# Kernel tuning notes

Measured on AMD Instinct MI355X. Metric: run time of the kernel, lower is better.

## Reference

```python
import jax, jax.numpy as jnp
import numpy as np

B, N, D = 16, 4096, 6
NUM_CENTERS, K = 1024, 32
EPS = 1e-5


def setup_inputs() -> dict:
    key = jax.random.key(0)
    ks = jax.random.split(key, 6)
    xyz = jax.random.uniform(ks[0], (B, N, 3), dtype=jnp.float32)
    features = jax.random.normal(ks[1], (B, N, D), dtype=jnp.float32)
    W1 = jax.random.normal(ks[2], (3 + D, 64), dtype=jnp.float32) * 0.1
    W2 = jax.random.normal(ks[3], (64, 64), dtype=jnp.float32) * 0.1
    W3 = jax.random.normal(ks[4], (64, 128), dtype=jnp.float32) * 0.1
    return {
        "xyz": xyz, "features": features,
        "W1": W1, "g1": jnp.ones((64,)), "b1": jnp.zeros((64,)),
        "W2": W2, "g2": jnp.ones((64,)), "b2": jnp.zeros((64,)),
        "W3": W3, "g3": jnp.ones((128,)), "b3": jnp.zeros((128,)),
    }


def square_distance(a, b):
    # a: [B,S,3], b: [B,N,3] -> [B,S,N] squared euclidean distance
    d2 = (jnp.sum(a * a, -1)[:, :, None]
          + jnp.sum(b * b, -1)[:, None, :]
          - 2.0 * jnp.einsum('bsc,bnc->bsn', a, b))
    return jnp.maximum(d2, 0.0)


def farthest_point_sample(xyz, num_centers):
    # xyz: [B,N,3] -> centers_idx: [B,S]. First center fixed at index 0
    # (original uses a random first index; deterministic here).
    Bn = xyz.shape[0]
    batch = jnp.arange(Bn)
    first = jnp.zeros((Bn,), jnp.int32)
    d0 = jnp.sum((xyz - xyz[batch, first][:, None, :]) ** 2, -1)  # [B,N]

    def step(dist_closest, _):
        idx = jnp.argmax(dist_closest, axis=1).astype(jnp.int32)  # [B]
        c = xyz[batch, idx]                                        # [B,3]
        d = jnp.sum((xyz - c[:, None, :]) ** 2, -1)                # [B,N]
        return jnp.minimum(dist_closest, d), idx

    _, rest = jax.lax.scan(step, d0, None, length=num_centers - 1)  # [S-1,B]
    return jnp.concatenate([first[:, None], rest.T], axis=1)        # [B,S]


def gather_bsk(points, idx):
    # points: [B,N,C], idx: [B,S,K] -> [B,S,K,C]
    Bn = points.shape[0]
    return points[jnp.arange(Bn)[:, None, None], idx]


def conv_bn_relu(x, W, g, b):
    # 1x1 conv (channel matmul) + training-mode BatchNorm (biased var) + ReLU
    x = jnp.einsum('bskc,co->bsko', x, W)
    m = jnp.mean(x, axis=(0, 1, 2))
    v = jnp.var(x, axis=(0, 1, 2))
    return jax.nn.relu((x - m) * jax.lax.rsqrt(v + EPS) * g + b)


def reference(xyz, features, W1, g1, b1, W2, g2, b2, W3, g3, b3):
    Bn = xyz.shape[0]
    batch = jnp.arange(Bn)
    centers_idx = farthest_point_sample(xyz, NUM_CENTERS)          # [B,S]
    centers_xyz = xyz[batch[:, None], centers_idx]                  # [B,S,3]

    # kNN grouping: [B,S,N] distance matrix, top-K smallest
    d2 = square_distance(centers_xyz, xyz)
    _, group_idx = jax.lax.top_k(-d2, K)                            # [B,S,K]

    group_xyz = gather_bsk(xyz, group_idx) - centers_xyz[:, :, None, :]
    group_feat = gather_bsk(features, group_idx)
    group = jnp.concatenate([group_xyz, group_feat], axis=-1)       # [B,S,K,3+D]

    x = conv_bn_relu(group, W1, g1, b1)
    x = conv_bn_relu(x, W2, g2, b2)
    x = conv_bn_relu(x, W3, g3, b3)
    centers_features = jnp.max(x, axis=2)                           # [B,S,C_out]
    return centers_xyz, centers_features
```

## Files before the change

kernel.cpp:

```cpp
#include <hip/hip_runtime.h>

#define BN_   16
#define NPTS  4096
#define DFEAT 6
#define SCTR  1024
#define KNN   32
#define RTOT  (BN_*SCTR*KNN)
#define EPSV  1e-5f
#define RNF   524288.0f
#define NREP  64

__device__ __forceinline__ float fmulx(float a, float b){ return __fmul_rn(a,b); }
__device__ __forceinline__ float faddx(float a, float b){ return __fadd_rn(a,b); }
__device__ __forceinline__ float fsubx(float a, float b){ return __fsub_rn(a,b); }
__device__ __forceinline__ float sq3x(float x, float y, float z){
  return faddx(faddx(fmulx(x,x), fmulx(y,y)), fmulx(z,z));
}
__device__ __forceinline__ float dot3fma(float ax, float ay, float az,
                                         float bx, float by, float bz){
  return __fmaf_rn(az, bz, __fmaf_rn(ay, by, __fmul_rn(ax, bx)));
}

__device__ __forceinline__ unsigned fkey(float f){
  unsigned u = __float_as_uint(f);
  return (u & 0x80000000u) ? ~u : (u | 0x80000000u);
}
__device__ __forceinline__ float funkey(unsigned k){
  return (k & 0x80000000u) ? __uint_as_float(k & 0x7fffffffu) : __uint_as_float(~k);
}

template<int CTRL>
__device__ __forceinline__ unsigned dpp_mv(unsigned v){
  return (unsigned)__builtin_amdgcn_update_dpp((int)v, (int)v, CTRL, 0xf, 0xf, false);
}
__device__ __forceinline__ unsigned wave_umax_b(unsigned v){
  unsigned o;
  o=dpp_mv<0x111>(v); v=v>o?v:o;
  o=dpp_mv<0x112>(v); v=v>o?v:o;
  o=dpp_mv<0x114>(v); v=v>o?v:o;
  o=dpp_mv<0x118>(v); v=v>o?v:o;
  o=dpp_mv<0x142>(v); v=v>o?v:o;
  o=dpp_mv<0x143>(v); v=v>o?v:o;
  return (unsigned)__builtin_amdgcn_readlane((int)v, 63);
}
__device__ __forceinline__ unsigned wave_umin_b(unsigned v){
  unsigned o;
  o=dpp_mv<0x111>(v); v=v<o?v:o;
  o=dpp_mv<0x112>(v); v=v<o?v:o;
  o=dpp_mv<0x114>(v); v=v<o?v:o;
  o=dpp_mv<0x118>(v); v=v<o?v:o;
  o=dpp_mv<0x142>(v); v=v<o?v:o;
  o=dpp_mv<0x143>(v); v=v<o?v:o;
  return (unsigned)__builtin_amdgcn_readlane((int)v, 63);
}

__global__ __launch_bounds__(256) void k_fps(const float* __restrict__ xyz,
                                             float* __restrict__ cxyz){
  const int b = blockIdx.x, tid = threadIdx.x;
  const int wave = tid>>6, lane = tid&63;
  const float* X = xyz + (size_t)b*NPTS*3;
  __shared__ float Xl[NPTS*3];
  __shared__ float Cl[SCTR*3];
  __shared__ unsigned long long slot[2][4];
  for(int i=tid;i<NPTS*3;i+=256) Xl[i]=X[i];
  __syncthreads();
  float px[16],py[16],pz[16],mind[16];
  const float c0x=Xl[0], c0y=Xl[1], c0z=Xl[2];
#pragma unroll
  for(int t=0;t<16;t++){
    const int j = lane + 64*(wave*16+t);
    px[t]=Xl[j*3]; py[t]=Xl[j*3+1]; pz[t]=Xl[j*3+2];
    mind[t]=sq3x(fsubx(px[t],c0x), fsubx(py[t],c0y), fsubx(pz[t],c0z));
  }
  if(tid==0){ Cl[0]=c0x; Cl[1]=c0y; Cl[2]=c0z; }
  float bv=-1.0f; int bj=0x7fffffff;
#pragma unroll
  for(int t=0;t<16;t++){
    const int j = lane + 64*(wave*16+t);
    if(mind[t]>bv){ bv=mind[t]; bj=j; }
  }
  for(int it=1; it<SCTR; ++it){
    const unsigned uv = __float_as_uint(bv);
    const unsigned M  = wave_umax_b(uv);
    const unsigned nj = (uv == M) ? ~(unsigned)bj : 0u;
    const unsigned NJ = wave_umax_b(nj);
    if(lane==0) slot[it&1][wave] = ((unsigned long long)M<<32) | NJ;
    __syncthreads();
    unsigned long long k0=slot[it&1][0], k1=slot[it&1][1],
                       k2=slot[it&1][2], k3=slot[it&1][3];
    unsigned long long ka = k0>k1?k0:k1;
    unsigned long long kb = k2>k3?k2:k3;
    unsigned long long kw = ka>kb?ka:kb;
    const int w = (int)(~(unsigned)kw);
    const float cx=Xl[w*3], cy=Xl[w*3+1], cz=Xl[w*3+2];
    if(tid==0){ Cl[it*3]=cx; Cl[it*3+1]=cy; Cl[it*3+2]=cz; }
    bv=-1.0f; bj=0x7fffffff;
#pragma unroll
    for(int t=0;t<16;t++){
      float d = sq3x(fsubx(px[t],cx), fsubx(py[t],cy), fsubx(pz[t],cz));
      float nm = fminf(mind[t], d);
      mind[t]=nm;
      const int j = lane + 64*(wave*16+t);
      if(nm>bv){ bv=nm; bj=j; }
    }
  }
  __syncthreads();
  float* O = cxyz + (size_t)b*SCTR*3;
  for(int i=tid;i<SCTR*3;i+=256) O[i]=Cl[i];
}

__global__ __launch_bounds__(256) void k_select(const float* __restrict__ xyz,
                                                const float* __restrict__ cxyz,
                                                int* __restrict__ gidx){
  const int lane = threadIdx.x & 63;
  const int cid  = blockIdx.x*4 + (threadIdx.x>>6);
  const int b = cid>>10;
  const float* X = xyz + (size_t)b*NPTS*3;
  const float* C = cxyz + (size_t)cid*3;
  const float cx=C[0], cy=C[1], cz=C[2];
  const float a2 = sq3x(cx,cy,cz);
  float d[64];
#pragma unroll
  for(int t=0;t<64;t++){
    int j = lane + (t<<6);
    float x=X[j*3], y=X[j*3+1], z=X[j*3+2];
    float b2 = sq3x(x,y,z);
    float dt = dot3fma(cx,cy,cz, x,y,z);
    float dd = fsubx(faddx(a2,b2), fmulx(2.0f,dt));
    d[t] = fmaxf(dd, 0.0f);
  }
  unsigned long long taken = 0ull;
  int* out = gidx + (size_t)cid*KNN;
#pragma unroll 1
  for(int r=0;r<KNN;r++){
    float mv = 3.0e38f; int mt = 63;
#pragma unroll
    for(int t=0;t<64;t++){
      if(!(taken & (1ull<<t)) && d[t] < mv){ mv = d[t]; mt = t; }
    }
    const unsigned um = __float_as_uint(mv);
    const unsigned Mw = wave_umin_b(um);
    const unsigned jc = (um == Mw) ? (unsigned)(lane + (mt<<6)) : 0xffffffffu;
    const unsigned WJ = wave_umin_b(jc);
    if(lane == (int)(WJ & 63u)){
      out[r] = (int)WJ;
      taken |= (1ull << (WJ >> 6));
    }
  }
}

__device__ __forceinline__ void stage_in(float* INt, int rbase,
                                         const float* __restrict__ xyz,
                                         const float* __restrict__ feat,
                                         const float* __restrict__ cxyz,
                                         const int* __restrict__ gidx){
  const int tid = threadIdx.x;
  const int row = tid>>2, sub = tid&3;
  const int r  = rbase + row;
  const int bb = r>>15, ss=(r>>5)&1023;
  const int idx = gidx[r];
  if(sub==0){
    const float* P = xyz  + ((size_t)bb*NPTS + idx)*3;
    const float* C = cxyz + ((size_t)(bb*SCTR)+ss)*3;
    INt[0*68+row] = P[0]-C[0];
    INt[1*68+row] = P[1]-C[1];
    INt[2*68+row] = P[2]-C[2];
  }else{
    const float* F = feat + ((size_t)bb*NPTS + idx)*6;
    const int c = (sub-1)*2;
    INt[(3+c)*68+row] = F[c];
    INt[(4+c)*68+row] = F[c+1];
  }
}

__device__ __forceinline__ void gemm1(const float* INt, const float* __restrict__ W1,
                                      int rt, int ct, float acc[4][4]){
#pragma unroll
  for(int i=0;i<4;i++)
#pragma unroll
    for(int j=0;j<4;j++) acc[i][j]=0.f;
#pragma unroll
  for(int c=0;c<9;c++){
    const float4 a = *(const float4*)&INt[c*68 + rt*4];
    const float4 w = *(const float4*)&W1[c*64 + ct*4];
    const float av[4]={a.x,a.y,a.z,a.w}, wv[4]={w.x,w.y,w.z,w.w};
#pragma unroll
    for(int i=0;i<4;i++)
#pragma unroll
      for(int j=0;j<4;j++) acc[i][j] += av[i]*wv[j];
  }
}

__device__ __forceinline__ float fold_rep(const float* __restrict__ pstats, int off){
  float s=0.f;
#pragma unroll 8
  for(int c=0;c<NREP;c++) s += pstats[c*512 + off];
  return s;
}

__global__ __launch_bounds__(256) void k_stats1(const float* __restrict__ xyz,
                                                const float* __restrict__ feat,
                                                const float* __restrict__ cxyz,
                                                const int* __restrict__ gidx,
                                                const float* __restrict__ W1,
                                                float* __restrict__ pstats){
  __shared__ __align__(16) float INt[9*68];
  __shared__ float sb[64], qb[64];
  const int tid=threadIdx.x;
  if(tid<64){ sb[tid]=0.f; qb[tid]=0.f; }
  stage_in(INt, blockIdx.x*64, xyz, feat, cxyz, gidx);
  __syncthreads();
  const int rt=tid&15, ct=tid>>4;
  float acc[4][4];
  gemm1(INt, W1, rt, ct, acc);
#pragma unroll
  for(int j=0;j<4;j++){
    float s=0.f, q=0.f;
#pragma unroll
    for(int i=0;i<4;i++){ float v=acc[i][j]; s+=v; q+=v*v; }
    atomicAdd(&sb[ct*4+j], s); atomicAdd(&qb[ct*4+j], q);
  }
  __syncthreads();
  if(tid<64){
    float* ps = pstats + (size_t)(blockIdx.x & (NREP-1))*512;
    atomicAdd(&ps[tid], sb[tid]); atomicAdd(&ps[64+tid], qb[tid]);
  }
}

template<bool WRITEZ>
__device__ __forceinline__ void stats2_body(const float* xyz, const float* feat,
                                            const float* cxyz, const int* gidx,
                                            const float* W1, const float* g1,
                                            const float* b1, const float* __restrict__ W2,
                                            float* pstats, float* Z2){
  __shared__ __align__(16) float INt[9*68];
  __shared__ __align__(16) float A1t[64*68];
  __shared__ float af1A[64], af1B[64];
  __shared__ float sb[64], qb[64];
  const int tid=threadIdx.x;
  if(tid<64){
    float sm = fold_rep(pstats, tid);
    float sq = fold_rep(pstats, 64+tid);
    float m  = sm/RNF;
    float vv = sq/RNF - m*m;
    float A  = rsqrtf(vv+EPSV)*g1[tid];
    af1A[tid]=A; af1B[tid]=b1[tid]-m*A;
    sb[tid]=0.f; qb[tid]=0.f;
  }
  stage_in(INt, blockIdx.x*64, xyz, feat, cxyz, gidx);
  __syncthreads();
  const int rt=tid&15, ct=tid>>4;
  float acc1[4][4];
  gemm1(INt, W1, rt, ct, acc1);
#pragma unroll
  for(int j=0;j<4;j++){
    const int o=ct*4+j; const float A=af1A[o], Bc=af1B[o];
#pragma unroll
    for(int i=0;i<4;i++) A1t[o*68 + rt*4+i] = fmaxf(acc1[i][j]*A+Bc, 0.f);
  }
  __syncthreads();
  float acc2[4][4];
#pragma unroll
  for(int i=0;i<4;i++)
#pragma unroll
    for(int j=0;j<4;j++) acc2[i][j]=0.f;
#pragma unroll
  for(int c=0;c<64;c++){
    const float4 a = *(const float4*)&A1t[c*68 + rt*4];
    const float4 w = *(const float4*)&W2[c*64 + ct*4];
    const float av[4]={a.x,a.y,a.z,a.w}, wv[4]={w.x,w.y,w.z,w.w};
#pragma unroll
    for(int i=0;i<4;i++)
#pragma unroll
      for(int j=0;j<4;j++) acc2[i][j] += av[i]*wv[j];
  }
  if(WRITEZ){
#pragma unroll
    for(int i=0;i<4;i++){
      float4 v = make_float4(acc2[i][0],acc2[i][1],acc2[i][2],acc2[i][3]);
      *(float4*)&Z2[((size_t)blockIdx.x*64 + rt*4+i)*64 + ct*4] = v;
    }
  }
#pragma unroll
  for(int j=0;j<4;j++){
    float s=0.f, q=0.f;
#pragma unroll
    for(int i=0;i<4;i++){ float v=acc2[i][j]; s+=v; q+=v*v; }
    atomicAdd(&sb[ct*4+j], s); atomicAdd(&qb[ct*4+j], q);
  }
  __syncthreads();
  if(tid<64){
    float* ps = pstats + (size_t)(blockIdx.x & (NREP-1))*512;
    atomicAdd(&ps[128+tid], sb[tid]); atomicAdd(&ps[192+tid], qb[tid]);
  }
}

__global__ __launch_bounds__(256) void k_stats2(const float* __restrict__ xyz,
                                                const float* __restrict__ feat,
                                                const float* __restrict__ cxyz,
                                                const int* __restrict__ gidx,
                                                const float* __restrict__ W1,
                                                const float* __restrict__ g1,
                                                const float* __restrict__ b1,
                                                const float* __restrict__ W2,
                                                float* __restrict__ pstats){
  stats2_body<false>(xyz,feat,cxyz,gidx,W1,g1,b1,W2,pstats,nullptr);
}
__global__ __launch_bounds__(256) void k_stats2m(const float* __restrict__ xyz,
                                                 const float* __restrict__ feat,
                                                 const float* __restrict__ cxyz,
                                                 const int* __restrict__ gidx,
                                                 const float* __restrict__ W1,
                                                 const float* __restrict__ g1,
                                                 const float* __restrict__ b1,
                                                 const float* __restrict__ W2,
                                                 float* __restrict__ pstats,
                                                 float* __restrict__ Z2){
  stats2_body<true>(xyz,feat,cxyz,gidx,W1,g1,b1,W2,pstats,Z2);
}

__global__ __launch_bounds__(256) void k_layer3(const float* __restrict__ xyz,
                                                const float* __restrict__ feat,
                                                const float* __restrict__ cxyz,
                                                const int* __restrict__ gidx,
                                                const float* __restrict__ W1,
                                                const float* __restrict__ g1,
                                                const float* __restrict__ b1,
                                                const float* __restrict__ W2,
                                                const float* __restrict__ g2,
                                                const float* __restrict__ b2,
                                                const float* __restrict__ W3,
                                                float* __restrict__ pstats,
                                                float* __restrict__ premax){
  __shared__ __align__(16) float INt[9*68];
  __shared__ __align__(16) float A1t[64*68];
  __shared__ float af1A[64], af1B[64], af2A[64], af2B[64];
  __shared__ unsigned mx[256];
  __shared__ float s3b[256], q3b[256];
  const int tid=threadIdx.x;
  if(tid<64){
    float sm = fold_rep(pstats, tid);
    float sq = fold_rep(pstats, 64+tid);
    float m  = sm/RNF;
    float vv = sq/RNF - m*m;
    float A  = rsqrtf(vv+EPSV)*g1[tid];
    af1A[tid]=A; af1B[tid]=b1[tid]-m*A;
    float sm2 = fold_rep(pstats, 128+tid);
    float sq2 = fold_rep(pstats, 192+tid);
    float m2 = sm2/RNF;
    float v2 = sq2/RNF - m2*m2;
    float A2 = rsqrtf(v2+EPSV)*g2[tid];
    af2A[tid]=A2; af2B[tid]=b2[tid]-m2*A2;
  }
  mx[tid]=0u; s3b[tid]=0.f; q3b[tid]=0.f;
  stage_in(INt, blockIdx.x*64, xyz, feat, cxyz, gidx);
  __syncthreads();
  const int rt=tid&15, ct=tid>>4;
  float acc1[4][4];
  gemm1(INt, W1, rt, ct, acc1);
#pragma unroll
  for(int j=0;j<4;j++){
    const int o=ct*4+j; const float A=af1A[o], Bc=af1B[o];
#pragma unroll
    for(int i=0;i<4;i++) A1t[o*68 + rt*4+i] = fmaxf(acc1[i][j]*A+Bc, 0.f);
  }
  __syncthreads();
  float acc2[4][4];
#pragma unroll
  for(int i=0;i<4;i++)
#pragma unroll
    for(int j=0;j<4;j++) acc2[i][j]=0.f;
#pragma unroll
  for(int c=0;c<64;c++){
    const float4 a = *(const float4*)&A1t[c*68 + rt*4];
    const float4 w = *(const float4*)&W2[c*64 + ct*4];
    const float av[4]={a.x,a.y,a.z,a.w}, wv[4]={w.x,w.y,w.z,w.w};
#pragma unroll
    for(int i=0;i<4;i++)
#pragma unroll
      for(int j=0;j<4;j++) acc2[i][j] += av[i]*wv[j];
  }
  float a2v[4][4];
#pragma unroll
  for(int j=0;j<4;j++){
    const int o=ct*4+j; const float A=af2A[o], Bc=af2B[o];
#pragma unroll
    for(int i=0;i<4;i++) a2v[i][j]=fmaxf(acc2[i][j]*A+Bc, 0.f);
  }
  __syncthreads();
#pragma unroll
  for(int j=0;j<4;j++)
#pragma unroll
    for(int i=0;i<4;i++) A1t[(ct*4+j)*68 + rt*4+i] = a2v[i][j];
  __syncthreads();
  float acc3[4][8];
#pragma unroll
  for(int i=0;i<4;i++)
#pragma unroll
    for(int j=0;j<8;j++) acc3[i][j]=0.f;
#pragma unroll
  for(int c=0;c<64;c++){
    const float4 a  = *(const float4*)&A1t[c*68 + rt*4];
    const float4 w0 = *(const float4*)&W3[c*128 + ct*8];
    const float4 w1 = *(const float4*)&W3[c*128 + ct*8 + 4];
    const float av[4]={a.x,a.y,a.z,a.w};
    const float wv[8]={w0.x,w0.y,w0.z,w0.w,w1.x,w1.y,w1.z,w1.w};
#pragma unroll
    for(int i=0;i<4;i++)
#pragma unroll
      for(int j=0;j<8;j++) acc3[i][j] += av[i]*wv[j];
  }
  const int g = rt>>3;
#pragma unroll
  for(int j=0;j<8;j++){
    const int o=ct*8+j;
    float lm=acc3[0][j], s=0.f, q=0.f;
#pragma unroll
    for(int i=0;i<4;i++){ float v=acc3[i][j]; lm=fmaxf(lm,v); s+=v; q+=v*v; }
    atomicMax(&mx[g*128+o], fkey(lm));
    atomicAdd(&s3b[g*128+o], s);
    atomicAdd(&q3b[g*128+o], q);
  }
  __syncthreads();
  {
    const int gg=tid>>7, o=tid&127;
    const int cid = blockIdx.x*2+gg;
    premax[(size_t)cid*128+o] = funkey(mx[tid]);
  }
  if(tid<128){
    float* ps = pstats + (size_t)(blockIdx.x & (NREP-1))*512;
    atomicAdd(&ps[256+tid], s3b[tid]+s3b[128+tid]);
    atomicAdd(&ps[384+tid], q3b[tid]+q3b[128+tid]);
  }
}

__global__ __launch_bounds__(256) void k_layer3z(const float* __restrict__ Z2,
                                                 const float* __restrict__ g2,
                                                 const float* __restrict__ b2,
                                                 const float* __restrict__ W3,
                                                 float* __restrict__ pstats,
                                                 float* __restrict__ premax){
  __shared__ __align__(16) float A2t[64*68];
  __shared__ float af2A[64], af2B[64];
  __shared__ unsigned mx[256];
  __shared__ float s3b[256], q3b[256];
  const int tid=threadIdx.x;
  if(tid<64){
    float sm2 = fold_rep(pstats, 128+tid);
    float sq2 = fold_rep(pstats, 192+tid);
    float m2 = sm2/RNF;
    float v2 = sq2/RNF - m2*m2;
    float A2 = rsqrtf(v2+EPSV)*g2[tid];
    af2A[tid]=A2; af2B[tid]=b2[tid]-m2*A2;
  }
  mx[tid]=0u; s3b[tid]=0.f; q3b[tid]=0.f;
  __syncthreads();
  {
    const int row = tid>>2, cq = (tid&3)*16;
    const float* zr = Z2 + ((size_t)blockIdx.x*64 + row)*64 + cq;
    const float4 z0 = *(const float4*)(zr);
    const float4 z1 = *(const float4*)(zr+4);
    const float4 z2 = *(const float4*)(zr+8);
    const float4 z3 = *(const float4*)(zr+12);
    const float zz[16]={z0.x,z0.y,z0.z,z0.w, z1.x,z1.y,z1.z,z1.w,
                        z2.x,z2.y,z2.z,z2.w, z3.x,z3.y,z3.z,z3.w};
#pragma unroll
    for(int u=0;u<16;u++){
      const int c = cq+u;
      A2t[c*68+row] = fmaxf(zz[u]*af2A[c]+af2B[c], 0.f);
    }
  }
  __syncthreads();
  const int rt=tid&15, ct=tid>>4;
  float acc3[4][8];
#pragma unroll
  for(int i=0;i<4;i++)
#pragma unroll
    for(int j=0;j<8;j++) acc3[i][j]=0.f;
#pragma unroll
  for(int c=0;c<64;c++){
    const float4 a  = *(const float4*)&A2t[c*68 + rt*4];
    const float4 w0 = *(const float4*)&W3[c*128 + ct*8];
    const float4 w1 = *(const float4*)&W3[c*128 + ct*8 + 4];
    const float av[4]={a.x,a.y,a.z,a.w};
    const float wv[8]={w0.x,w0.y,w0.z,w0.w,w1.x,w1.y,w1.z,w1.w};
#pragma unroll
    for(int i=0;i<4;i++)
#pragma unroll
      for(int j=0;j<8;j++) acc3[i][j] += av[i]*wv[j];
  }
  const int g = rt>>3;
#pragma unroll
  for(int j=0;j<8;j++){
    const int o=ct*8+j;
    float lm=acc3[0][j], s=0.f, q=0.f;
#pragma unroll
    for(int i=0;i<4;i++){ float v=acc3[i][j]; lm=fmaxf(lm,v); s+=v; q+=v*v; }
    atomicMax(&mx[g*128+o], fkey(lm));
    atomicAdd(&s3b[g*128+o], s);
    atomicAdd(&q3b[g*128+o], q);
  }
  __syncthreads();
  {
    const int gg=tid>>7, o=tid&127;
    const int cid = blockIdx.x*2+gg;
    premax[(size_t)cid*128+o] = funkey(mx[tid]);
  }
  if(tid<128){
    float* ps = pstats + (size_t)(blockIdx.x & (NREP-1))*512;
    atomicAdd(&ps[256+tid], s3b[tid]+s3b[128+tid]);
    atomicAdd(&ps[384+tid], q3b[tid]+q3b[128+tid]);
  }
}

__global__ __launch_bounds__(256) void k_red3(const float* __restrict__ pstats,
                                              float* __restrict__ cstats){
  const int t = threadIdx.x;
  cstats[t] = fold_rep(pstats, 256+t);
}

__global__ __launch_bounds__(256) void k_final(const float* __restrict__ cstats,
                                               const float* __restrict__ g3,
                                               const float* __restrict__ b3,
                                               float* __restrict__ outf){
  const int i = blockIdx.x*256 + threadIdx.x;
  const int o = i & 127;
  float m  = cstats[o]/RNF;
  float vv = cstats[128+o]/RNF - m*m;
  float A  = rsqrtf(vv+EPSV)*g3[o];
  float Bc = b3[o]-m*A;
  float v  = outf[i];
  outf[i] = fmaxf(v*A+Bc, 0.f);
}

extern "C" void kernel_launch(void* const* d_in, const int* in_sizes, int n_in,
                              void* d_out, int out_size, void* d_ws, size_t ws_size,
                              hipStream_t stream){
  const float* xyz  = (const float*)d_in[0];
  const float* feat = (const float*)d_in[1];
  const float* W1   = (const float*)d_in[2];
  const float* g1   = (const float*)d_in[3];
  const float* b1   = (const float*)d_in[4];
  const float* W2   = (const float*)d_in[5];
  const float* g2   = (const float*)d_in[6];
  const float* b2   = (const float*)d_in[7];
  const float* W3   = (const float*)d_in[8];
  const float* g3   = (const float*)d_in[9];
  const float* b3   = (const float*)d_in[10];
  float* out  = (float*)d_out;
  float* cxyz = out;
  float* outf = out + 16*1024*3;
  float* pstats = (float*)d_ws;
  float* cstats = (float*)((char*)d_ws + 131072);
  int*   gidx   = (int*)((char*)d_ws + 133120);
  float* Z2     = (float*)((char*)d_ws + 133120 + (size_t)RTOT*4);
  const size_t need = 133120 + (size_t)RTOT*4 + (size_t)RTOT*64*4;
  const bool fast = (ws_size >= need);

  hipMemsetAsync(pstats, 0, (size_t)NREP*512*sizeof(float), stream);
  k_fps   <<<16,   256,  0, stream>>>(xyz, cxyz);
  k_select<<<4096, 256,  0, stream>>>(xyz, cxyz, gidx);
  k_stats1<<<8192, 256,  0, stream>>>(xyz, feat, cxyz, gidx, W1, pstats);
  if(fast){
    k_stats2m<<<8192, 256, 0, stream>>>(xyz, feat, cxyz, gidx, W1, g1, b1, W2, pstats, Z2);
    k_layer3z<<<8192, 256, 0, stream>>>(Z2, g2, b2, W3, pstats, outf);
  }else{
    k_stats2 <<<8192, 256, 0, stream>>>(xyz, feat, cxyz, gidx, W1, g1, b1, W2, pstats);
    k_layer3 <<<8192, 256, 0, stream>>>(xyz, feat, cxyz, gidx, W1, g1, b1, W2, g2, b2, W3, pstats, outf);
  }
  k_red3  <<<1,    256,  0, stream>>>(pstats, cstats);
  k_final <<<8192, 256,  0, stream>>>(cstats, g3, b3, outf);
}
```

Baseline: 1.667 ms.

## Widen FPS to 512 threads and use quarter-cached minima in kNN selection

The farthest-point-sampling kernel now runs 8 waves per batch instead of 4, so each lane holds 8 points rather than 16 and the serial 1023-iteration loop does half the per-lane distance work, at the cost of an 8-way cross-wave reduction. The kNN selection kernel keeps a cached minimum for each of four 16-entry quarters of the per-lane distance array. Each round only compares those four values, and only the winning lane rescans the quarter it took from, instead of every lane scanning all 64 entries every round. This reduces per-round ALU work but adds divergent rescans and more register state.

```diff
diff --git a/kernel.cpp b/kernel.cpp
--- a/kernel.cpp
+++ b/kernel.cpp
@@ -54,29 +54,29 @@
   return (unsigned)__builtin_amdgcn_readlane((int)v, 63);
 }
 
-__global__ __launch_bounds__(256) void k_fps(const float* __restrict__ xyz,
+__global__ __launch_bounds__(512) void k_fps(const float* __restrict__ xyz,
                                              float* __restrict__ cxyz){
   const int b = blockIdx.x, tid = threadIdx.x;
   const int wave = tid>>6, lane = tid&63;
   const float* X = xyz + (size_t)b*NPTS*3;
   __shared__ float Xl[NPTS*3];
   __shared__ float Cl[SCTR*3];
-  __shared__ unsigned long long slot[2][4];
-  for(int i=tid;i<NPTS*3;i+=256) Xl[i]=X[i];
-  __syncthreads();
-  float px[16],py[16],pz[16],mind[16];
+  __shared__ unsigned long long slot[2][8];
+  for(int i=tid;i<NPTS*3;i+=512) Xl[i]=X[i];
+  __syncthreads();
+  float px[8],py[8],pz[8],mind[8];
   const float c0x=Xl[0], c0y=Xl[1], c0z=Xl[2];
 #pragma unroll
-  for(int t=0;t<16;t++){
-    const int j = lane + 64*(wave*16+t);
+  for(int t=0;t<8;t++){
+    const int j = lane + 64*(wave*8+t);
     px[t]=Xl[j*3]; py[t]=Xl[j*3+1]; pz[t]=Xl[j*3+2];
     mind[t]=sq3x(fsubx(px[t],c0x), fsubx(py[t],c0y), fsubx(pz[t],c0z));
   }
   if(tid==0){ Cl[0]=c0x; Cl[1]=c0y; Cl[2]=c0z; }
   float bv=-1.0f; int bj=0x7fffffff;
 #pragma unroll
-  for(int t=0;t<16;t++){
-    const int j = lane + 64*(wave*16+t);
+  for(int t=0;t<8;t++){
+    const int j = lane + 64*(wave*8+t);
     if(mind[t]>bv){ bv=mind[t]; bj=j; }
   }
   for(int it=1; it<SCTR; ++it){
@@ -86,27 +86,32 @@
     const unsigned NJ = wave_umax_b(nj);
     if(lane==0) slot[it&1][wave] = ((unsigned long long)M<<32) | NJ;
     __syncthreads();
-    unsigned long long k0=slot[it&1][0], k1=slot[it&1][1],
-                       k2=slot[it&1][2], k3=slot[it&1][3];
-    unsigned long long ka = k0>k1?k0:k1;
-    unsigned long long kb = k2>k3?k2:k3;
-    unsigned long long kw = ka>kb?ka:kb;
+    const unsigned long long* sp = slot[it&1];
+    const unsigned long long s0=sp[0], s1=sp[1], s2=sp[2], s3=sp[3],
+                             s4=sp[4], s5=sp[5], s6=sp[6], s7=sp[7];
+    unsigned long long ka = s0>s1?s0:s1;
+    unsigned long long kb = s2>s3?s2:s3;
+    unsigned long long kc = s4>s5?s4:s5;
+    unsigned long long kd = s6>s7?s6:s7;
+    unsigned long long ke = ka>kb?ka:kb;
+    unsigned long long kf = kc>kd?kc:kd;
+    unsigned long long kw = ke>kf?ke:kf;
     const int w = (int)(~(unsigned)kw);
     const float cx=Xl[w*3], cy=Xl[w*3+1], cz=Xl[w*3+2];
     if(tid==0){ Cl[it*3]=cx; Cl[it*3+1]=cy; Cl[it*3+2]=cz; }
     bv=-1.0f; bj=0x7fffffff;
 #pragma unroll
-    for(int t=0;t<16;t++){
-      float d = sq3x(fsubx(px[t],cx), fsubx(py[t],cy), fsubx(pz[t],cz));
-      float nm = fminf(mind[t], d);
+    for(int t=0;t<8;t++){
+      float dd = sq3x(fsubx(px[t],cx), fsubx(py[t],cy), fsubx(pz[t],cz));
+      float nm = fminf(mind[t], dd);
       mind[t]=nm;
-      const int j = lane + 64*(wave*16+t);
+      const int j = lane + 64*(wave*8+t);
       if(nm>bv){ bv=nm; bj=j; }
     }
   }
   __syncthreads();
   float* O = cxyz + (size_t)b*SCTR*3;
-  for(int i=tid;i<SCTR*3;i+=256) O[i]=Cl[i];
+  for(int i=tid;i<SCTR*3;i+=512) O[i]=Cl[i];
 }
 
 __global__ __launch_bounds__(256) void k_select(const float* __restrict__ xyz,
@@ -129,23 +134,49 @@
     float dd = fsubx(faddx(a2,b2), fmulx(2.0f,dt));
     d[t] = fmaxf(dd, 0.0f);
   }
+  float q0v=3.0e38f, q1v=3.0e38f, q2v=3.0e38f, q3v=3.0e38f;
+  int   q0t=0, q1t=16, q2t=32, q3t=48;
+#pragma unroll
+  for(int k=0;k<16;k++){ if(d[k]    < q0v){ q0v=d[k];    q0t=k;    } }
+#pragma unroll
+  for(int k=0;k<16;k++){ if(d[16+k] < q1v){ q1v=d[16+k]; q1t=16+k; } }
+#pragma unroll
+  for(int k=0;k<16;k++){ if(d[32+k] < q2v){ q2v=d[32+k]; q2t=32+k; } }
+#pragma unroll
+  for(int k=0;k<16;k++){ if(d[48+k] < q3v){ q3v=d[48+k]; q3t=48+k; } }
   unsigned long long taken = 0ull;
   int* out = gidx + (size_t)cid*KNN;
 #pragma unroll 1
   for(int r=0;r<KNN;r++){
-    float mv = 3.0e38f; int mt = 63;
-#pragma unroll
-    for(int t=0;t<64;t++){
-      if(!(taken & (1ull<<t)) && d[t] < mv){ mv = d[t]; mt = t; }
-    }
+    float mv = q0v; int mt = q0t;
+    if(q1v < mv){ mv=q1v; mt=q1t; }
+    if(q2v < mv){ mv=q2v; mt=q2t; }
+    if(q3v < mv){ mv=q3v; mt=q3t; }
     const unsigned um = __float_as_uint(mv);
     const unsigned Mw = wave_umin_b(um);
     const unsigned jc = (um == Mw) ? (unsigned)(lane + (mt<<6)) : 0xffffffffu;
     const unsigned WJ = wave_umin_b(jc);
-    if(lane == (int)(WJ & 63u)){
+    const int wl = (int)(WJ & 63u);
+    const int wt = (int)(WJ >> 6);
+    if(lane == wl){
       out[r] = (int)WJ;
-      taken |= (1ull << (WJ >> 6));
+      taken |= (1ull << wt);
     }
+    const int wq = wt >> 4;
+#define RESCAN_Q(QV,QT,BASE) \
+    if(lane == wl){ \
+      float nv=3.0e38f; int nt=BASE; \
+      _Pragma("unroll") \
+      for(int k2=0;k2<16;k2++){ \
+        if(!(taken & (1ull<<(BASE+k2))) && d[BASE+k2] < nv){ nv=d[BASE+k2]; nt=BASE+k2; } \
+      } \
+      QV=nv; QT=nt; \
+    }
+    if(wq==0)      { RESCAN_Q(q0v,q0t,0)  }
+    else if(wq==1) { RESCAN_Q(q1v,q1t,16) }
+    else if(wq==2) { RESCAN_Q(q2v,q2t,32) }
+    else           { RESCAN_Q(q3v,q3t,48) }
+#undef RESCAN_Q
   }
 }
 
@@ -558,7 +589,7 @@
   const bool fast = (ws_size >= need);
 
   hipMemsetAsync(pstats, 0, (size_t)NREP*512*sizeof(float), stream);
-  k_fps   <<<16,   256,  0, stream>>>(xyz, cxyz);
+  k_fps   <<<16,   512,  0, stream>>>(xyz, cxyz);
   k_select<<<4096, 256,  0, stream>>>(xyz, cxyz, gidx);
   k_stats1<<<8192, 256,  0, stream>>>(xyz, feat, cxyz, gidx, W1, pstats);
   if(fast){
```

Result: faster. 1.555 ms (-6.7%).

## Cache per-quarter minima in kNN select, DPP stat reductions, precompute BN coefficients

Applied to the files above, without the earlier changes.

The kNN selection now keeps four per-lane quarter minima and, after each pick, rescans only the quarter that lost an element. The old code rescanned all 64 candidates on every one of the 32 rounds. Per-block batch-norm sum and sum-of-squares reductions replace LDS atomics with DPP row reductions across the 16 row-threads. BN affine coefficients are computed once in a tiny k_coef kernel instead of every block folding 64 replicas of the partial stats. This adds two small kernel launches and a divergent rescan branch in the select loop.

```diff
diff --git a/kernel.cpp b/kernel.cpp
--- a/kernel.cpp
+++ b/kernel.cpp
@@ -52,6 +52,15 @@
   o=dpp_mv<0x142>(v); v=v<o?v:o;
   o=dpp_mv<0x143>(v); v=v<o?v:o;
   return (unsigned)__builtin_amdgcn_readlane((int)v, 63);
+}
+
+__device__ __forceinline__ float row16_sum(float x){
+  float s = x;
+  s += __int_as_float(__builtin_amdgcn_update_dpp(0, __float_as_int(s), 0x111, 0xf, 0xf, true));
+  s += __int_as_float(__builtin_amdgcn_update_dpp(0, __float_as_int(s), 0x112, 0xf, 0xf, true));
+  s += __int_as_float(__builtin_amdgcn_update_dpp(0, __float_as_int(s), 0x114, 0xf, 0xf, true));
+  s += __int_as_float(__builtin_amdgcn_update_dpp(0, __float_as_int(s), 0x118, 0xf, 0xf, true));
+  return s;
 }
 
 __global__ __launch_bounds__(256) void k_fps(const float* __restrict__ xyz,
@@ -129,23 +138,49 @@
     float dd = fsubx(faddx(a2,b2), fmulx(2.0f,dt));
     d[t] = fmaxf(dd, 0.0f);
   }
+  float q0v=3.0e38f, q1v=3.0e38f, q2v=3.0e38f, q3v=3.0e38f;
+  int   q0t=0, q1t=16, q2t=32, q3t=48;
+#pragma unroll
+  for(int k=0;k<16;k++){ if(d[k]    < q0v){ q0v=d[k];    q0t=k;    } }
+#pragma unroll
+  for(int k=0;k<16;k++){ if(d[16+k] < q1v){ q1v=d[16+k]; q1t=16+k; } }
+#pragma unroll
+  for(int k=0;k<16;k++){ if(d[32+k] < q2v){ q2v=d[32+k]; q2t=32+k; } }
+#pragma unroll
+  for(int k=0;k<16;k++){ if(d[48+k] < q3v){ q3v=d[48+k]; q3t=48+k; } }
   unsigned long long taken = 0ull;
   int* out = gidx + (size_t)cid*KNN;
 #pragma unroll 1
   for(int r=0;r<KNN;r++){
-    float mv = 3.0e38f; int mt = 63;
-#pragma unroll
-    for(int t=0;t<64;t++){
-      if(!(taken & (1ull<<t)) && d[t] < mv){ mv = d[t]; mt = t; }
-    }
+    float mv = q0v; int mt = q0t;
+    if(q1v < mv){ mv=q1v; mt=q1t; }
+    if(q2v < mv){ mv=q2v; mt=q2t; }
+    if(q3v < mv){ mv=q3v; mt=q3t; }
     const unsigned um = __float_as_uint(mv);
     const unsigned Mw = wave_umin_b(um);
     const unsigned jc = (um == Mw) ? (unsigned)(lane + (mt<<6)) : 0xffffffffu;
     const unsigned WJ = wave_umin_b(jc);
-    if(lane == (int)(WJ & 63u)){
+    const int wl = (int)(WJ & 63u);
+    const int wt = (int)(WJ >> 6);
+    if(lane == wl){
       out[r] = (int)WJ;
-      taken |= (1ull << (WJ >> 6));
+      taken |= (1ull << wt);
     }
+    const int wq = wt >> 4;
+#define RESCAN_Q(QV,QT,BASE) \
+    if(lane == wl){ \
+      float nv=3.0e38f; int nt=BASE; \
+      _Pragma("unroll") \
+      for(int k2=0;k2<16;k2++){ \
+        if(!(taken & (1ull<<(BASE+k2))) && d[BASE+k2] < nv){ nv=d[BASE+k2]; nt=BASE+k2; } \
+      } \
+      QV=nv; QT=nt; \
+    }
+    if(wq==0)      { RESCAN_Q(q0v,q0t,0)  }
+    else if(wq==1) { RESCAN_Q(q1v,q1t,16) }
+    else if(wq==2) { RESCAN_Q(q2v,q2t,32) }
+    else           { RESCAN_Q(q3v,q3t,48) }
+#undef RESCAN_Q
   }
 }
 
@@ -198,6 +233,21 @@
   return s;
 }
 
+__global__ __launch_bounds__(64) void k_coef(const float* __restrict__ pstats,
+                                             const float* __restrict__ g,
+                                             const float* __restrict__ b,
+                                             float* __restrict__ coefo,
+                                             int off){
+  const int t = threadIdx.x;
+  float sm = fold_rep(pstats, off+t);
+  float sq = fold_rep(pstats, off+64+t);
+  float m  = sm/RNF;
+  float vv = sq/RNF - m*m;
+  float A  = rsqrtf(vv+EPSV)*g[t];
+  coefo[t]    = A;
+  coefo[64+t] = b[t]-m*A;
+}
+
 __global__ __launch_bounds__(256) void k_stats1(const float* __restrict__ xyz,
                                                 const float* __restrict__ feat,
                                                 const float* __restrict__ cxyz,
@@ -207,7 +257,6 @@
   __shared__ __align__(16) float INt[9*68];
   __shared__ float sb[64], qb[64];
   const int tid=threadIdx.x;
-  if(tid<64){ sb[tid]=0.f; qb[tid]=0.f; }
   stage_in(INt, blockIdx.x*64, xyz, feat, cxyz, gidx);
   __syncthreads();
   const int rt=tid&15, ct=tid>>4;
@@ -218,7 +267,8 @@
     float s=0.f, q=0.f;
 #pragma unroll
     for(int i=0;i<4;i++){ float v=acc[i][j]; s+=v; q+=v*v; }
-    atomicAdd(&sb[ct*4+j], s); atomicAdd(&qb[ct*4+j], q);
+    s = row16_sum(s); q = row16_sum(q);
+    if(rt==15){ sb[ct*4+j]=s; qb[ct*4+j]=q; }
   }
   __syncthreads();
   if(tid<64){
@@ -230,8 +280,9 @@
 template<bool WRITEZ>
 __device__ __forceinline__ void stats2_body(const float* xyz, const float* feat,
                                             const float* cxyz, const int* gidx,
-                                            const float* W1, const float* g1,
-                                            const float* b1, const float* __restrict__ W2,
+                                            const float* W1,
+                                            const float* __restrict__ coef,
+                                            const float* __restrict__ W2,
                                             float* pstats, float* Z2){
   __shared__ __align__(16) float INt[9*68];
   __shared__ __align__(16) float A1t[64*68];
@@ -239,13 +290,7 @@
   __shared__ float sb[64], qb[64];
   const int tid=threadIdx.x;
   if(tid<64){
-    float sm = fold_rep(pstats, tid);
-    float sq = fold_rep(pstats, 64+tid);
-    float m  = sm/RNF;
-    float vv = sq/RNF - m*m;
-    float A  = rsqrtf(vv+EPSV)*g1[tid];
-    af1A[tid]=A; af1B[tid]=b1[tid]-m*A;
-    sb[tid]=0.f; qb[tid]=0.f;
+    af1A[tid]=coef[tid]; af1B[tid]=coef[64+tid];
   }
   stage_in(INt, blockIdx.x*64, xyz, feat, cxyz, gidx);
   __syncthreads();
@@ -286,7 +331,8 @@
     float s=0.f, q=0.f;
 #pragma unroll
     for(int i=0;i<4;i++){ float v=acc2[i][j]; s+=v; q+=v*v; }
-    atomicAdd(&sb[ct*4+j], s); atomicAdd(&qb[ct*4+j], q);
+    s = row16_sum(s); q = row16_sum(q);
+    if(rt==15){ sb[ct*4+j]=s; qb[ct*4+j]=q; }
   }
   __syncthreads();
   if(tid<64){
@@ -300,23 +346,21 @@
                                                 const float* __restrict__ cxyz,
                                                 const int* __restrict__ gidx,
                                                 const float* __restrict__ W1,
-                                                const float* __restrict__ g1,
-                                                const float* __restrict__ b1,
+                                                const float* __restrict__ coef,
                                                 const float* __restrict__ W2,
                                                 float* __restrict__ pstats){
-  stats2_body<false>(xyz,feat,cxyz,gidx,W1,g1,b1,W2,pstats,nullptr);
+  stats2_body<false>(xyz,feat,cxyz,gidx,W1,coef,W2,pstats,nullptr);
 }
 __global__ __launch_bounds__(256) void k_stats2m(const float* __restrict__ xyz,
                                                  const float* __restrict__ feat,
                                                  const float* __restrict__ cxyz,
                                                  const int* __restrict__ gidx,
                                                  const float* __restrict__ W1,
-                                                 const float* __restrict__ g1,
-                                                 const float* __restrict__ b1,
+                                                 const float* __restrict__ coef,
                                                  const float* __restrict__ W2,
                                                  float* __restrict__ pstats,
                                                  float* __restrict__ Z2){
-  stats2_body<true>(xyz,feat,cxyz,gidx,W1,g1,b1,W2,pstats,Z2);
+  stats2_body<true>(xyz,feat,cxyz,gidx,W1,coef,W2,pstats,Z2);
 }
 
 __global__ __launch_bounds__(256) void k_layer3(const float* __restrict__ xyz,
@@ -324,11 +368,8 @@
                                                 const float* __restrict__ cxyz,
                                                 const int* __restrict__ gidx,
                                                 const float* __restrict__ W1,
-                                                const float* __restrict__ g1,
-                                                const float* __restrict__ b1,
+                                                const float* __restrict__ coef,
                                                 const float* __restrict__ W2,
-                                                const float* __restrict__ g2,
-                                                const float* __restrict__ b2,
                                                 const float* __restrict__ W3,
                                                 float* __restrict__ pstats,
                                                 float* __restrict__ premax){
@@ -336,23 +377,13 @@
   __shared__ __align__(16) float A1t[64*68];
   __shared__ float af1A[64], af1B[64], af2A[64], af2B[64];
   __shared__ unsigned mx[256];
-  __shared__ float s3b[256], q3b[256];
+  __shared__ float s3b[128], q3b[128];
   const int tid=threadIdx.x;
   if(tid<64){
-    float sm = fold_rep(pstats, tid);
-    float sq = fold_rep(pstats, 64+tid);
-    float m  = sm/RNF;
-    float vv = sq/RNF - m*m;
-    float A  = rsqrtf(vv+EPSV)*g1[tid];
-    af1A[tid]=A; af1B[tid]=b1[tid]-m*A;
-    float sm2 = fold_rep(pstats, 128+tid);
-    float sq2 = fold_rep(pstats, 192+tid);
-    float m2 = sm2/RNF;
-    float v2 = sq2/RNF - m2*m2;
-    float A2 = rsqrtf(v2+EPSV)*g2[tid];
-    af2A[tid]=A2; af2B[tid]=b2[tid]-m2*A2;
-  }
-  mx[tid]=0u; s3b[tid]=0.f; q3b[tid]=0.f;
+    af1A[tid]=coef[tid];     af1B[tid]=coef[64+tid];
+    af2A[tid]=coef[128+tid]; af2B[tid]=coef[192+tid];
+  }
+  mx[tid]=0u;
   stage_in(INt, blockIdx.x*64, xyz, feat, cxyz, gidx);
   __syncthreads();
   const int rt=tid&15, ct=tid>>4;
@@ -418,8 +449,8 @@
 #pragma unroll
     for(int i=0;i<4;i++){ float v=acc3[i][j]; lm=fmaxf(lm,v); s+=v; q+=v*v; }
     atomicMax(&mx[g*128+o], fkey(lm));
-    atomicAdd(&s3b[g*128+o], s);
-    atomicAdd(&q3b[g*128+o], q);
+    s = row16_sum(s); q = row16_sum(q);
+    if(rt==15){ s3b[o]=s; q3b[o]=q; }
   }
   __syncthreads();
   {
@@ -429,31 +460,25 @@
   }
   if(tid<128){
     float* ps = pstats + (size_t)(blockIdx.x & (NREP-1))*512;
-    atomicAdd(&ps[256+tid], s3b[tid]+s3b[128+tid]);
-    atomicAdd(&ps[384+tid], q3b[tid]+q3b[128+tid]);
+    atomicAdd(&ps[256+tid], s3b[tid]);
+    atomicAdd(&ps[384+tid], q3b[tid]);
   }
 }
 
 __global__ __launch_bounds__(256) void k_layer3z(const float* __restrict__ Z2,
-                                                 const float* __restrict__ g2,
-                                                 const float* __restrict__ b2,
+                                                 const float* __restrict__ coef,
                                                  const float* __restrict__ W3,
                                                  float* __restrict__ pstats,
                                                  float* __restrict__ premax){
   __shared__ __align__(16) float A2t[64*68];
   __shared__ float af2A[64], af2B[64];
   __shared__ unsigned mx[256];
-  __shared__ float s3b[256], q3b[256];
+  __shared__ float s3b[128], q3b[128];
   const int tid=threadIdx.x;
   if(tid<64){
-    float sm2 = fold_rep(pstats, 128+tid);
-    float sq2 = fold_rep(pstats, 192+tid);
-    float m2 = sm2/RNF;
-    float v2 = sq2/RNF - m2*m2;
-    float A2 = rsqrtf(v2+EPSV)*g2[tid];
-    af2A[tid]=A2; af2B[tid]=b2[tid]-m2*A2;
-  }
-  mx[tid]=0u; s3b[tid]=0.f; q3b[tid]=0.f;
+    af2A[tid]=coef[128+tid]; af2B[tid]=coef[192+tid];
+  }
+  mx[tid]=0u;
   __syncthreads();
   {
     const int row = tid>>2, cq = (tid&3)*16;
@@ -497,8 +522,8 @@
 #pragma unroll
     for(int i=0;i<4;i++){ float v=acc3[i][j]; lm=fmaxf(lm,v); s+=v; q+=v*v; }
     atomicMax(&mx[g*128+o], fkey(lm));
-    atomicAdd(&s3b[g*128+o], s);
-    atomicAdd(&q3b[g*128+o], q);
+    s = row16_sum(s); q = row16_sum(q);
+    if(rt==15){ s3b[o]=s; q3b[o]=q; }
   }
   __syncthreads();
   {
@@ -508,8 +533,8 @@
   }
   if(tid<128){
     float* ps = pstats + (size_t)(blockIdx.x & (NREP-1))*512;
-    atomicAdd(&ps[256+tid], s3b[tid]+s3b[128+tid]);
-    atomicAdd(&ps[384+tid], q3b[tid]+q3b[128+tid]);
+    atomicAdd(&ps[256+tid], s3b[tid]);
+    atomicAdd(&ps[384+tid], q3b[tid]);
   }
 }
 
@@ -552,6 +577,7 @@
   float* outf = out + 16*1024*3;
   float* pstats = (float*)d_ws;
   float* cstats = (float*)((char*)d_ws + 131072);
+  float* coef   = (float*)((char*)d_ws + 132096);
   int*   gidx   = (int*)((char*)d_ws + 133120);
   float* Z2     = (float*)((char*)d_ws + 133120 + (size_t)RTOT*4);
   const size_t need = 133120 + (size_t)RTOT*4 + (size_t)RTOT*64*4;
@@ -561,12 +587,15 @@
   k_fps   <<<16,   256,  0, stream>>>(xyz, cxyz);
   k_select<<<4096, 256,  0, stream>>>(xyz, cxyz, gidx);
   k_stats1<<<8192, 256,  0, stream>>>(xyz, feat, cxyz, gidx, W1, pstats);
+  k_coef  <<<1,    64,   0, stream>>>(pstats, g1, b1, coef, 0);
   if(fast){
-    k_stats2m<<<8192, 256, 0, stream>>>(xyz, feat, cxyz, gidx, W1, g1, b1, W2, pstats, Z2);
-    k_layer3z<<<8192, 256, 0, stream>>>(Z2, g2, b2, W3, pstats, outf);
+    k_stats2m<<<8192, 256, 0, stream>>>(xyz, feat, cxyz, gidx, W1, coef, W2, pstats, Z2);
+    k_coef  <<<1,    64,  0, stream>>>(pstats, g2, b2, coef+128, 128);
+    k_layer3z<<<8192, 256, 0, stream>>>(Z2, coef, W3, pstats, outf);
   }else{
-    k_stats2 <<<8192, 256, 0, stream>>>(xyz, feat, cxyz, gidx, W1, g1, b1, W2, pstats);
-    k_layer3 <<<8192, 256, 0, stream>>>(xyz, feat, cxyz, gidx, W1, g1, b1, W2, g2, b2, W3, pstats, outf);
+    k_stats2 <<<8192, 256, 0, stream>>>(xyz, feat, cxyz, gidx, W1, coef, W2, pstats);
+    k_coef  <<<1,    64,  0, stream>>>(pstats, g2, b2, coef+128, 128);
+    k_layer3 <<<8192, 256, 0, stream>>>(xyz, feat, cxyz, gidx, W1, coef, W2, W3, pstats, outf);
   }
   k_red3  <<<1,    256,  0, stream>>>(pstats, cstats);
   k_final <<<8192, 256,  0, stream>>>(cstats, g3, b3, outf);
```

After: 4.983 ms. 2.99x slower.
